# Optimization experiments

Measured on AMD Instinct MI355X. Metric: run time of the kernel, lower is better.

The kernel has to match this reference:

```python
import jax, jax.numpy as jnp
import numpy as np


def setup_inputs() -> dict:
    key = jax.random.key(0)
    ks = jax.random.split(key, 8)
    n_states, n_hidden, bs = 64, 256, 256
    return {
        "z0": jax.random.normal(ks[0], (bs, n_states), jnp.float32),
        "A": jax.random.uniform(ks[1], (n_states,), jnp.float32),  # stable diagonal
        "W1": jax.random.normal(ks[2], (n_hidden, n_states), jnp.float32) * (1.0 / np.sqrt(n_hidden)),
        "W2": jax.random.normal(ks[3], (n_states, n_hidden), jnp.float32) * (1.0 / np.sqrt(n_states)),
        "h1": jax.random.normal(ks[4], (n_states,), jnp.float32),
        "h2": jax.random.normal(ks[5], (n_hidden,), jnp.float32),
        "OB": jax.random.normal(ks[6], (n_states, n_states), jnp.float32) * (1.0 / np.sqrt(n_states)),
        "Ob": jax.random.normal(ks[7], (n_states,), jnp.float32),
        "nt": 4096,
    }


def reference(z0, A, W1, W2, h1, h2, OB, Ob, nt):
    # Clipped shallow PLRNN recurrence:
    # z_{t+1} = A*z_t + (relu(z_t@W2 + h2) - relu(z_t@W2)) @ W1 + h1
    def step(z, _):
        W2z = z @ W2  # [bs, n_hidden]
        z_new = A * z + (jax.nn.relu(W2z + h2) - jax.nn.relu(W2z)) @ W1 + h1
        return z_new, z_new

    _, zs = jax.lax.scan(step, z0, None, length=nt)  # [nt, bs, n_states]
    z = jnp.concatenate([z0[:, None, :], jnp.moveaxis(zs, 0, 1)], axis=1)  # [bs, nt+1, n_states]
    x = z @ OB + Ob  # observation
    return x
```

## Files before the change

### kernel.cpp

```cpp
#include <hip/hip_runtime.h>


#define NS 64
#define NH 256
#define BS 256

typedef float v2f __attribute__((ext_vector_type(2)));

#define PIN(x) asm volatile("" : "+v"(x))

__device__ __forceinline__ float dppx1(float x) {
    return __int_as_float(__builtin_amdgcn_mov_dpp(__float_as_int(x), 0xB1, 0xF, 0xF, true));
}
__device__ __forceinline__ float dppx2(float x) {
    return __int_as_float(__builtin_amdgcn_mov_dpp(__float_as_int(x), 0x4E, 0xF, 0xF, true));
}
__device__ __forceinline__ float dppror8(float x) {
    return __int_as_float(__builtin_amdgcn_mov_dpp(__float_as_int(x), 0x128, 0xF, 0xF, true));
}

__global__ __launch_bounds__(256) __attribute__((amdgpu_waves_per_eu(1, 1)))
void plrnn_kernel(const float* __restrict__ z0,
                  const float* __restrict__ A,
                  const float* __restrict__ W1,
                  const float* __restrict__ W2,
                  const float* __restrict__ h1,
                  const float* __restrict__ h2,
                  const float* __restrict__ OB,
                  const float* __restrict__ Ob,
                  const int* __restrict__ ntp,
                  float* __restrict__ X)
{
    const int b    = blockIdx.x;
    const int tid  = threadIdx.x;
    const int g    = tid >> 2;
    const int s    = tid & 3;
    const int w    = tid >> 6;
    const int lane = tid & 63;
    const int nt   = *ntp;
    const bool s1  = (s & 1) != 0;
    const bool s2b = (s & 2) != 0;

    const int b0 = lane & 1, b1 = (lane >> 1) & 1, b2 = (lane >> 2) & 1;
    const int b4 = (lane >> 4) & 1;
    const bool bb0 = b0 != 0, bb1 = b1 != 0;
    const int S2 = b0 | (b1 << 1) | (((lane >> 3) & 1) << 2) | (((lane >> 5) & 1) << 3);
    const int obase  = 16 * w + 4 * (b2 | (b4 << 1));
    const int o_lane = obase + 2 * b1 + b0;

    __shared__ __align__(16) float zsh[NS];
    __shared__ __align__(16) float phish[4 * 68];

    v2f w2p[4][8];
    #pragma unroll
    for (int k2 = 0; k2 < 8; ++k2) {
        const int r0 = 16 * s + 2 * k2;
        const float4 a0 = *reinterpret_cast<const float4*>(&W2[(r0 + 0) * NH + 4 * g]);
        const float4 a1 = *reinterpret_cast<const float4*>(&W2[(r0 + 1) * NH + 4 * g]);
        w2p[0][k2] = (v2f){a0.x, a1.x};
        w2p[1][k2] = (v2f){a0.y, a1.y};
        w2p[2][k2] = (v2f){a0.z, a1.z};
        w2p[3][k2] = (v2f){a0.w, a1.w};
    }
    v2f w1p[4][8];
    #pragma unroll
    for (int t2 = 0; t2 < 8; ++t2) {
        const int r0 = 16 * S2 + 2 * t2;
        const float4 a0 = *reinterpret_cast<const float4*>(&W1[(r0 + 0) * NS + obase]);
        const float4 a1 = *reinterpret_cast<const float4*>(&W1[(r0 + 1) * NS + obase]);
        w1p[0][t2] = (v2f){a0.x, a1.x};
        w1p[1][t2] = (v2f){a0.y, a1.y};
        w1p[2][t2] = (v2f){a0.z, a1.z};
        w1p[3][t2] = (v2f){a0.w, a1.w};
    }
    v2f obp[8];
    #pragma unroll
    for (int k2 = 0; k2 < 8; ++k2)
        obp[k2] = (v2f){OB[(16 * s + 2 * k2) * NS + g], OB[(16 * s + 2 * k2 + 1) * NS + g]};

    #pragma unroll
    for (int j = 0; j < 4; ++j) {
        #pragma unroll
        for (int k = 0; k < 8; ++k) { PIN(w2p[j][k]); PIN(w1p[j][k]); }
    }
    #pragma unroll
    for (int k = 0; k < 8; ++k) PIN(obp[k]);

    const float hA  = A[o_lane];
    const float hh1 = h1[o_lane];
    const float hh2 = h2[tid];
    const float hOb = Ob[g];
    float zcur = z0[b * NS + o_lane];

    if (tid < NS) zsh[tid] = z0[b * NS + tid];
    __syncthreads();

    float* __restrict__ Xb = X + (size_t)b * (size_t)(nt + 1) * NS;
    const float4* zs4  = reinterpret_cast<const float4*>(zsh) + 4 * s;
    const float4* ph4b = reinterpret_cast<const float4*>(phish + 68 * (S2 >> 2) + 16 * (S2 & 3));

    for (int t = 0; t < nt; ++t) {
        const float4 za = zs4[0], zb = zs4[1], zc = zs4[2], zd = zs4[3];
        const v2f zz2[8] = {{za.x, za.y}, {za.z, za.w}, {zb.x, zb.y}, {zb.z, zb.w},
                            {zc.x, zc.y}, {zc.z, zc.w}, {zd.x, zd.y}, {zd.z, zd.w}};

        v2f q0 = {0.f, 0.f}, q1 = {0.f, 0.f}, q2 = {0.f, 0.f}, q3 = {0.f, 0.f};
        #pragma unroll
        for (int k2 = 0; k2 < 8; ++k2) {
            q0 = __builtin_elementwise_fma(zz2[k2], w2p[0][k2], q0);
            q1 = __builtin_elementwise_fma(zz2[k2], w2p[1][k2], q1);
            q2 = __builtin_elementwise_fma(zz2[k2], w2p[2][k2], q2);
            q3 = __builtin_elementwise_fma(zz2[k2], w2p[3][k2], q3);
        }
        const float p0 = q0.x + q0.y, p1 = q1.x + q1.y, p2 = q2.x + q2.y, p3 = q3.x + q3.y;

        v2f xop = {0.f, 0.f};
        #pragma unroll
        for (int k2 = 0; k2 < 8; ++k2) xop = __builtin_elementwise_fma(zz2[k2], obp[k2], xop);

        float sA = s1 ? p0 : p1;  float rA = dppx1(sA);  float k0 = (s1 ? p1 : p0) + rA;
        float sB = s1 ? p2 : p3;  float rB = dppx1(sB);  float k1 = (s1 ? p3 : p2) + rB;
        float sC = s2b ? k0 : k1; float rC = dppx2(sC);  float W2z = (s2b ? k1 : k0) + rC;

        const float ph = fmaxf(W2z + hh2, 0.f) - fmaxf(W2z, 0.f);
        phish[w * 68 + lane] = ph;

        float xr = xop.x + xop.y;
        xr += dppx1(xr);
        xr += dppx2(xr);
        if (s == 0) Xb[(size_t)t * NS + g] = xr + hOb;

        __syncthreads();

        const float4 f0 = ph4b[0], f1 = ph4b[1], f2 = ph4b[2], f3 = ph4b[3];
        const v2f ff[8] = {{f0.x, f0.y}, {f0.z, f0.w}, {f1.x, f1.y}, {f1.z, f1.w},
                           {f2.x, f2.y}, {f2.z, f2.w}, {f3.x, f3.y}, {f3.z, f3.w}};
        v2f u0 = {0.f, 0.f}, u1 = {0.f, 0.f}, u2 = {0.f, 0.f}, u3 = {0.f, 0.f};
        #pragma unroll
        for (int t2 = 0; t2 < 8; ++t2) {
            u0 = __builtin_elementwise_fma(ff[t2], w1p[0][t2], u0);
            u1 = __builtin_elementwise_fma(ff[t2], w1p[1][t2], u1);
            u2 = __builtin_elementwise_fma(ff[t2], w1p[2][t2], u2);
            u3 = __builtin_elementwise_fma(ff[t2], w1p[3][t2], u3);
        }
        const float v0 = u0.x + u0.y, v1 = u1.x + u1.y, v2 = u2.x + u2.y, v3 = u3.x + u3.y;

        float tA = bb0 ? v0 : v1;  float wA = dppx1(tA);  float kA = (bb0 ? v1 : v0) + wA;
        float tB = bb0 ? v2 : v3;  float wB = dppx1(tB);  float kB = (bb0 ? v3 : v2) + wB;
        float tC = bb1 ? kA : kB;  float wC = dppx2(tC);  float P  = (bb1 ? kB : kA) + wC;
        P += dppror8(P);
        P += __shfl_xor(P, 32);

        zcur = fmaf(hA, zcur, P + hh1);
        if ((lane & 40) == 0) zsh[o_lane] = zcur;

        __syncthreads();
    }

    {
        const float4 za = zs4[0], zb = zs4[1], zc = zs4[2], zd = zs4[3];
        const v2f zz2[8] = {{za.x, za.y}, {za.z, za.w}, {zb.x, zb.y}, {zb.z, zb.w},
                            {zc.x, zc.y}, {zc.z, zc.w}, {zd.x, zd.y}, {zd.z, zd.w}};
        v2f xop = {0.f, 0.f};
        #pragma unroll
        for (int k2 = 0; k2 < 8; ++k2) xop = __builtin_elementwise_fma(zz2[k2], obp[k2], xop);
        float xr = xop.x + xop.y;
        xr += dppx1(xr);
        xr += dppx2(xr);
        if (s == 0) Xb[(size_t)nt * NS + g] = xr + hOb;
    }
}

extern "C" void kernel_launch(void* const* d_in, const int* in_sizes, int n_in,
                              void* d_out, int out_size, void* d_ws, size_t ws_size,
                              hipStream_t stream) {
    const float* z0 = (const float*)d_in[0];
    const float* A  = (const float*)d_in[1];
    const float* W1 = (const float*)d_in[2];
    const float* W2 = (const float*)d_in[3];
    const float* h1 = (const float*)d_in[4];
    const float* h2 = (const float*)d_in[5];
    const float* OB = (const float*)d_in[6];
    const float* Ob = (const float*)d_in[7];
    const int*   ntp = (const int*)d_in[8];
    float* X = (float*)d_out;

    plrnn_kernel<<<BS, 256, 0, stream>>>(z0, A, W1, W2, h1, h2, OB, Ob, ntp, X);
}
```

Baseline: 2.126 ms.

## Replace second-stage cross-wave reduction with per-wave partials and one barrier per step

Changes the W1 work split so each wave handles 64 of the 256 hidden units for all 64 outputs. Each wave writes its partial sums to a double-buffered shared array, and the four partials are combined after a single barrier. Every wave keeps its own copy of z and phi in shared memory, so the first barrier per step becomes a wave-local lgkmcnt wait. The goal is to halve the block-wide barriers in the serial recurrence. In exchange, every wave redundantly computes the z update, and the correctness of the wave-local waits depends on in-wave LDS ordering.

New measurement: 2.180 ms. 1.03x slower.

```diff
diff --git a/kernel.cpp b/kernel.cpp
--- a/kernel.cpp
+++ b/kernel.cpp
@@ -8,15 +8,14 @@
 typedef float v2f __attribute__((ext_vector_type(2)));
 
 #define PIN(x) asm volatile("" : "+v"(x))
+#define LGKM0() asm volatile("s_waitcnt lgkmcnt(0)" ::: "memory")
+#define BAR()   asm volatile("s_waitcnt lgkmcnt(0)\ns_barrier" ::: "memory")
 
 __device__ __forceinline__ float dppx1(float x) {
     return __int_as_float(__builtin_amdgcn_mov_dpp(__float_as_int(x), 0xB1, 0xF, 0xF, true));
 }
 __device__ __forceinline__ float dppx2(float x) {
     return __int_as_float(__builtin_amdgcn_mov_dpp(__float_as_int(x), 0x4E, 0xF, 0xF, true));
-}
-__device__ __forceinline__ float dppror8(float x) {
-    return __int_as_float(__builtin_amdgcn_mov_dpp(__float_as_int(x), 0x128, 0xF, 0xF, true));
 }
 
 __global__ __launch_bounds__(256) __attribute__((amdgpu_waves_per_eu(1, 1)))
@@ -37,19 +36,14 @@
     const int s    = tid & 3;
     const int w    = tid >> 6;
     const int lane = tid & 63;
+    const int o4   = lane >> 2;
     const int nt   = *ntp;
     const bool s1  = (s & 1) != 0;
     const bool s2b = (s & 2) != 0;
 
-    const int b0 = lane & 1, b1 = (lane >> 1) & 1, b2 = (lane >> 2) & 1;
-    const int b4 = (lane >> 4) & 1;
-    const bool bb0 = b0 != 0, bb1 = b1 != 0;
-    const int S2 = b0 | (b1 << 1) | (((lane >> 3) & 1) << 2) | (((lane >> 5) & 1) << 3);
-    const int obase  = 16 * w + 4 * (b2 | (b4 << 1));
-    const int o_lane = obase + 2 * b1 + b0;
-
-    __shared__ __align__(16) float zsh[NS];
-    __shared__ __align__(16) float phish[4 * 68];
+    __shared__ __align__(16) float zsh[4][72];
+    __shared__ __align__(16) float phiL[4][72];
+    __shared__ __align__(16) float part[2][4][68];
 
     v2f w2p[4][8];
     #pragma unroll
@@ -65,9 +59,9 @@
     v2f w1p[4][8];
     #pragma unroll
     for (int t2 = 0; t2 < 8; ++t2) {
-        const int r0 = 16 * S2 + 2 * t2;
-        const float4 a0 = *reinterpret_cast<const float4*>(&W1[(r0 + 0) * NS + obase]);
-        const float4 a1 = *reinterpret_cast<const float4*>(&W1[(r0 + 1) * NS + obase]);
+        const int r0 = 64 * w + 16 * s + 2 * t2;
+        const float4 a0 = *reinterpret_cast<const float4*>(&W1[(r0 + 0) * NS + 4 * o4]);
+        const float4 a1 = *reinterpret_cast<const float4*>(&W1[(r0 + 1) * NS + 4 * o4]);
         w1p[0][t2] = (v2f){a0.x, a1.x};
         w1p[1][t2] = (v2f){a0.y, a1.y};
         w1p[2][t2] = (v2f){a0.z, a1.z};
@@ -86,20 +80,22 @@
     #pragma unroll
     for (int k = 0; k < 8; ++k) PIN(obp[k]);
 
-    const float hA  = A[o_lane];
-    const float hh1 = h1[o_lane];
+    const float hA  = A[lane];
+    const float hh1 = h1[lane];
     const float hh2 = h2[tid];
     const float hOb = Ob[g];
-    float zcur = z0[b * NS + o_lane];
+    float zcur = z0[b * NS + lane];
 
-    if (tid < NS) zsh[tid] = z0[b * NS + tid];
-    __syncthreads();
+    zsh[w][lane] = zcur;
+    LGKM0();
 
     float* __restrict__ Xb = X + (size_t)b * (size_t)(nt + 1) * NS;
-    const float4* zs4  = reinterpret_cast<const float4*>(zsh) + 4 * s;
-    const float4* ph4b = reinterpret_cast<const float4*>(phish + 68 * (S2 >> 2) + 16 * (S2 & 3));
+    const float4* zs4 = reinterpret_cast<const float4*>(&zsh[w][16 * s]);
+    const float4* ph4 = reinterpret_cast<const float4*>(&phiL[w][16 * s]);
 
     for (int t = 0; t < nt; ++t) {
+        const int pb = t & 1;
+
         const float4 za = zs4[0], zb = zs4[1], zc = zs4[2], zd = zs4[3];
         const v2f zz2[8] = {{za.x, za.y}, {za.z, za.w}, {zb.x, zb.y}, {zb.z, zb.w},
                             {zc.x, zc.y}, {zc.z, zc.w}, {zd.x, zd.y}, {zd.z, zd.w}};
@@ -114,25 +110,24 @@
         }
         const float p0 = q0.x + q0.y, p1 = q1.x + q1.y, p2 = q2.x + q2.y, p3 = q3.x + q3.y;
 
-        v2f xop = {0.f, 0.f};
-        #pragma unroll
-        for (int k2 = 0; k2 < 8; ++k2) xop = __builtin_elementwise_fma(zz2[k2], obp[k2], xop);
-
         float sA = s1 ? p0 : p1;  float rA = dppx1(sA);  float k0 = (s1 ? p1 : p0) + rA;
         float sB = s1 ? p2 : p3;  float rB = dppx1(sB);  float k1 = (s1 ? p3 : p2) + rB;
         float sC = s2b ? k0 : k1; float rC = dppx2(sC);  float W2z = (s2b ? k1 : k0) + rC;
 
         const float ph = fmaxf(W2z + hh2, 0.f) - fmaxf(W2z, 0.f);
-        phish[w * 68 + lane] = ph;
+        phiL[w][lane] = ph;
 
+        v2f xop = {0.f, 0.f};
+        #pragma unroll
+        for (int k2 = 0; k2 < 8; ++k2) xop = __builtin_elementwise_fma(zz2[k2], obp[k2], xop);
         float xr = xop.x + xop.y;
         xr += dppx1(xr);
         xr += dppx2(xr);
         if (s == 0) Xb[(size_t)t * NS + g] = xr + hOb;
 
-        __syncthreads();
+        LGKM0();
 
-        const float4 f0 = ph4b[0], f1 = ph4b[1], f2 = ph4b[2], f3 = ph4b[3];
+        const float4 f0 = ph4[0], f1 = ph4[1], f2 = ph4[2], f3 = ph4[3];
         const v2f ff[8] = {{f0.x, f0.y}, {f0.z, f0.w}, {f1.x, f1.y}, {f1.z, f1.w},
                            {f2.x, f2.y}, {f2.z, f2.w}, {f3.x, f3.y}, {f3.z, f3.w}};
         v2f u0 = {0.f, 0.f}, u1 = {0.f, 0.f}, u2 = {0.f, 0.f}, u3 = {0.f, 0.f};
@@ -145,16 +140,22 @@
         }
         const float v0 = u0.x + u0.y, v1 = u1.x + u1.y, v2 = u2.x + u2.y, v3 = u3.x + u3.y;
 
-        float tA = bb0 ? v0 : v1;  float wA = dppx1(tA);  float kA = (bb0 ? v1 : v0) + wA;
-        float tB = bb0 ? v2 : v3;  float wB = dppx1(tB);  float kB = (bb0 ? v3 : v2) + wB;
-        float tC = bb1 ? kA : kB;  float wC = dppx2(tC);  float P  = (bb1 ? kB : kA) + wC;
-        P += dppror8(P);
-        P += __shfl_xor(P, 32);
+        float tA = s1 ? v0 : v1;  float wA = dppx1(tA);  float kA = (s1 ? v1 : v0) + wA;
+        float tB = s1 ? v2 : v3;  float wB = dppx1(tB);  float kB = (s1 ? v3 : v2) + wB;
+        float tC = s2b ? kA : kB; float wC = dppx2(tC);  float Pp = (s2b ? kB : kA) + wC;
 
-        zcur = fmaf(hA, zcur, P + hh1);
-        if ((lane & 40) == 0) zsh[o_lane] = zcur;
+        part[pb][w][lane] = Pp;
 
-        __syncthreads();
+        BAR();
+
+        const float c0 = part[pb][0][lane];
+        const float c1 = part[pb][1][lane];
+        const float c2 = part[pb][2][lane];
+        const float c3 = part[pb][3][lane];
+
+        zcur = fmaf(hA, zcur, (c0 + c1) + (c2 + c3) + hh1);
+        zsh[w][lane] = zcur;
+        LGKM0();
     }
 
     {
```
